# Kernel tuning notes

Measured on AMD Instinct MI355X. Metric: run time of the kernel, lower is better.

Reference implementation:

```python
import jax, jax.numpy as jnp
import numpy as np

NEG_INF = -9e15


def setup_inputs() -> dict:
    key = jax.random.key(0)
    k1, k2, k3, k4, k5 = jax.random.split(key, 5)
    N, F_IN, F_OUT = 8192, 512, 256
    x = jax.random.normal(k1, (N, F_IN), dtype=jnp.float32)
    adjacent_matrix = jax.random.randint(k2, (N, N), 0, 2, dtype=jnp.int32)
    # xavier-normal-like scales (gain sqrt(2))
    W = jax.random.normal(k3, (F_IN, F_OUT), dtype=jnp.float32) * np.sqrt(2.0) * np.sqrt(2.0 / (F_IN + F_OUT))
    a1 = jax.random.normal(k4, (F_OUT, 1), dtype=jnp.float32) * np.sqrt(2.0) * np.sqrt(2.0 / (F_OUT + 1))
    a2 = jax.random.normal(k5, (F_OUT, 1), dtype=jnp.float32) * np.sqrt(2.0) * np.sqrt(2.0 / (F_OUT + 1))
    return {"x": x, "adjacent_matrix": adjacent_matrix, "W": W, "a1": a1, "a2": a2}


def reference(x, adjacent_matrix, W, a1, a2):
    alpha = 0.2  # LeakyReLU negative slope
    h = x @ W                                   # [N, F_out]
    f1 = h @ a1                                 # [N, 1]
    f2 = h @ a2                                 # [N, 1]
    e = f1 + f2.T                               # [N, N] broadcast pairwise scores
    e = jnp.where(e > 0, e, alpha * e)          # LeakyReLU
    e = jnp.where(adjacent_matrix > 0, e, NEG_INF)  # mask non-edges
    attention = jax.nn.softmax(e, axis=1)       # [N, N]
    h_prime = attention @ h                     # [N, F_out]
    return jax.nn.elu(h_prime)                  # concat=True -> ELU
```

## Files before the change

### kernel.cpp

```cpp
#include <hip/hip_runtime.h>
#include <hip/hip_bf16.h>

#define N_NODES 8192
#define F_IN 512
#define F_OUT 256
#define KSPLIT 4
#define KCHUNK (N_NODES / KSPLIT)
#define NTILES (KCHUNK / 32)

using short8 = __attribute__((ext_vector_type(8))) short;
using f32x4  = __attribute__((ext_vector_type(4))) float;

typedef __attribute__((address_space(3))) void lds_t;
typedef const __attribute__((address_space(1))) void gbl_t;

__device__ __forceinline__ short f2bf(float v) {
    union { float f; unsigned u; } x; x.f = v;
    unsigned r = x.u + 0x7fffu + ((x.u >> 16) & 1u);
    return (short)(r >> 16);
}

__global__ void k_prep(const float* __restrict__ W, const float* __restrict__ a1,
                       const float* __restrict__ a2, float* __restrict__ w1,
                       float* __restrict__ w2, short* __restrict__ WTg) {
    const int k = blockIdx.x;
    const int l = threadIdx.x;
    float4 wv = *(const float4*)(W + (size_t)k * F_OUT + 4 * l);
    float4 av = *(const float4*)(a1 + 4 * l);
    float4 bv = *(const float4*)(a2 + 4 * l);
    float s1 = wv.x*av.x + wv.y*av.y + wv.z*av.z + wv.w*av.w;
    float s2 = wv.x*bv.x + wv.y*bv.y + wv.z*bv.z + wv.w*bv.w;
    WTg[(size_t)(4*l+0)*F_IN + k] = f2bf(wv.x);
    WTg[(size_t)(4*l+1)*F_IN + k] = f2bf(wv.y);
    WTg[(size_t)(4*l+2)*F_IN + k] = f2bf(wv.z);
    WTg[(size_t)(4*l+3)*F_IN + k] = f2bf(wv.w);
    #pragma unroll
    for (int off = 32; off; off >>= 1) {
        s1 += __shfl_down(s1, off);
        s2 += __shfl_down(s2, off);
    }
    if (l == 0) { w1[k] = s1; w2[k] = s2; }
}

__global__ void k_f12(const float* __restrict__ x, const float* __restrict__ w1,
                      const float* __restrict__ w2, float* __restrict__ f1,
                      float* __restrict__ f2) {
    const int wv = threadIdx.x >> 6, l = threadIdx.x & 63;
    const int i = blockIdx.x * 4 + wv;
    const float* xr = x + (size_t)i * F_IN;
    float s1 = 0.f, s2 = 0.f;
    #pragma unroll
    for (int t = 0; t < 2; ++t) {
        int k = t * 256 + l * 4;
        float4 xv = *(const float4*)(xr + k);
        float4 u  = *(const float4*)(w1 + k);
        float4 v  = *(const float4*)(w2 + k);
        s1 += xv.x*u.x + xv.y*u.y + xv.z*u.z + xv.w*u.w;
        s2 += xv.x*v.x + xv.y*v.y + xv.z*v.z + xv.w*v.w;
    }
    #pragma unroll
    for (int off = 32; off; off >>= 1) {
        s1 += __shfl_down(s1, off);
        s2 += __shfl_down(s2, off);
    }
    if (l == 0) { f1[i] = s1; f2[i] = s2; }
}

__launch_bounds__(256)
__global__ void k_hT(const float* __restrict__ x, const short* __restrict__ WTg,
                     short* __restrict__ hT) {
    __shared__ short x_lds[32 * 64];
    __shared__ short wt_lds[256 * 64];
    const int tid = threadIdx.x;
    const int wv = tid >> 6, l = tid & 63, lg = l >> 4, lr = l & 15;
    const int ibase = blockIdx.x * 32;
    f32x4 acc[4][2];
    #pragma unroll
    for (int a = 0; a < 4; ++a)
        #pragma unroll
        for (int b = 0; b < 2; ++b) acc[a][b] = (f32x4){0.f, 0.f, 0.f, 0.f};
    for (int k0 = 0; k0 < F_IN; k0 += 64) {
        __syncthreads();
        {
            int i = tid >> 3, ch = tid & 7;
            const float* src = x + (size_t)(ibase + i) * F_IN + k0 + ch * 8;
            float4 v0 = *(const float4*)(src);
            float4 v1 = *(const float4*)(src + 4);
            short8 s;
            s[0]=f2bf(v0.x); s[1]=f2bf(v0.y); s[2]=f2bf(v0.z); s[3]=f2bf(v0.w);
            s[4]=f2bf(v1.x); s[5]=f2bf(v1.y); s[6]=f2bf(v1.z); s[7]=f2bf(v1.w);
            *(short8*)&x_lds[i * 64 + 8 * (ch ^ (i & 7))] = s;
        }
        {
            int cb = tid >> 3, ch = tid & 7;
            #pragma unroll
            for (int p = 0; p < 8; ++p) {
                int c = cb + 32 * p;
                short8 s = *(const short8*)(WTg + (size_t)c * F_IN + k0 + ch * 8);
                *(short8*)&wt_lds[c * 64 + 8 * (ch ^ (c & 7))] = s;
            }
        }
        __syncthreads();
        #pragma unroll
        for (int ks = 0; ks < 2; ++ks) {
            short8 bfrag[2], afrag[4];
            #pragma unroll
            for (int it = 0; it < 2; ++it) {
                int i = it * 16 + lr;
                bfrag[it] = *(short8*)&x_lds[i * 64 + 8 * ((lg + 4*ks) ^ (i & 7))];
            }
            #pragma unroll
            for (int ct = 0; ct < 4; ++ct) {
                int c = wv * 64 + ct * 16 + lr;
                afrag[ct] = *(short8*)&wt_lds[c * 64 + 8 * ((lg + 4*ks) ^ (c & 7))];
            }
            #pragma unroll
            for (int ct = 0; ct < 4; ++ct)
                #pragma unroll
                for (int it = 0; it < 2; ++it)
                    acc[ct][it] = __builtin_amdgcn_mfma_f32_16x16x32_bf16(
                        afrag[ct], bfrag[it], acc[ct][it], 0, 0, 0);
        }
    }
    #pragma unroll
    for (int ct = 0; ct < 4; ++ct)
        #pragma unroll
        for (int it = 0; it < 2; ++it)
            #pragma unroll
            for (int r = 0; r < 4; ++r) {
                int c = wv * 64 + ct * 16 + 4 * lg + r;
                int i = ibase + it * 16 + lr;
                hT[(size_t)c * N_NODES + i] = f2bf(acc[ct][it][r]);
            }
}

__launch_bounds__(256, 2)
__global__ void k_attn(const int* __restrict__ adj, const short* __restrict__ hT,
                       const float* __restrict__ f1, const float* __restrict__ f2,
                       float* __restrict__ part, float* __restrict__ psum) {
    __shared__ short h_lds[4 * 8192];
    __shared__ float f2_lds[KCHUNK];
    const int tid = threadIdx.x;
    const int wv = tid >> 6, l = tid & 63, lg = l >> 4, lr = l & 15;
    const int ksid = blockIdx.x & 3;
    const int rowblk = blockIdx.x >> 2;
    const int r0 = rowblk * 64;
    const int myrow = r0 + wv * 16 + lr;
    const int kbeg = ksid * KCHUNK;
    const short* hsrcb = hT + (size_t)(wv * 16 + (l >> 2)) * N_NODES
                            + ((l & 3) ^ ((l >> 3) & 3)) * 8 + kbeg;
    const int q = l & 3, srow = wv * 16 + (l >> 2);
    const int* asrcb = adj + (size_t)(r0 + srow) * N_NODES + q * 8 + kbeg;
    const float f1v = f1[myrow];
    const float L2E = 1.44269504f;
    const int rdoff = lr * 32 + (lg ^ ((lr >> 1) & 3)) * 8;
    f32x4 acc[16];
    #pragma unroll
    for (int t = 0; t < 16; ++t) acc[t] = (f32x4){0.f, 0.f, 0.f, 0.f};
    float ps = 0.f;

    int4 S0[2], S1[2], S2[2], S3[2];
    unsigned mA, mB;

#define STAGE(T) do {                                                           \
    _Pragma("unroll")                                                           \
    for (int p = 0; p < 4; ++p)                                                 \
        __builtin_amdgcn_global_load_lds(                                       \
            (gbl_t*)(hsrcb + (size_t)p * 64 * N_NODES + (T) * 32),              \
            (lds_t*)&h_lds[((T) & 3) * 8192 + p * 2048 + wv * 512], 16, 0, 0);  \
} while (0)

#define ADJ(S, T) do {                                                          \
    S[0] = *(const int4*)(asrcb + (T) * 32);                                    \
    S[1] = *(const int4*)(asrcb + (T) * 32 + 4);                                \
} while (0)

#define PACK(MD, S) do {                                                        \
    unsigned _m = (S[0].x > 0 ? 1u : 0u) | (S[0].y > 0 ? 2u : 0u) |             \
                  (S[0].z > 0 ? 4u : 0u) | (S[0].w > 0 ? 8u : 0u) |             \
                  (S[1].x > 0 ? 16u : 0u) | (S[1].y > 0 ? 32u : 0u) |           \
                  (S[1].z > 0 ? 64u : 0u) | (S[1].w > 0 ? 128u : 0u);           \
    MD = (unsigned)__shfl((int)_m, (lr << 2) | lg);                             \
} while (0)

#define COMPUTE(T, MB) do {                                                     \
    const int bo = ((T) & 3) * 8192;                                            \
    const float4 fa = *(const float4*)&f2_lds[(T) * 32 + lg * 8];               \
    const float4 fb4 = *(const float4*)&f2_lds[(T) * 32 + lg * 8 + 4];          \
    const float f2v[8] = {fa.x, fa.y, fa.z, fa.w, fb4.x, fb4.y, fb4.z, fb4.w};  \
    short8 pa;                                                                  \
    _Pragma("unroll")                                                           \
    for (int j = 0; j < 8; ++j) {                                               \
        float ee = f1v + f2v[j];                                                \
        float le = fmaxf(ee, 0.2f * ee);                                        \
        float pv = ((MB) & (1u << j)) ? exp2f(fminf(le * L2E, 80.f)) : 0.f;     \
        ps += pv;                                                               \
        pa[j] = f2bf(pv);                                                       \
    }                                                                           \
    __builtin_amdgcn_s_setprio(1);                                              \
    _Pragma("unroll")                                                           \
    for (int t16 = 0; t16 < 16; ++t16) {                                        \
        short8 bfrag = *(short8*)&h_lds[bo + t16 * 512 + rdoff];                \
        acc[t16] = __builtin_amdgcn_mfma_f32_16x16x32_bf16(pa, bfrag, acc[t16], 0, 0, 0); \
    }                                                                           \
    __builtin_amdgcn_s_setprio(0);                                              \
} while (0)

#define BODY(T, SL, SP, MU, MP) do {                                            \
    PACK(MP, SP);                                        \
    if ((T) + 4 < NTILES) ADJ(SL, (T) + 4);                                     \
    if ((T) + 2 < NTILES) STAGE((T) + 2);                                       \
    asm volatile("s_waitcnt vmcnt(12)" ::: "memory");                           \
    __builtin_amdgcn_s_barrier();                                               \
    __builtin_amdgcn_sched_barrier(0);                                          \
    COMPUTE(T, MU);                                                             \
} while (0)

    {
        int i8 = tid * 8;
        *(float4*)&f2_lds[i8]     = *(const float4*)(f2 + kbeg + i8);
        *(float4*)&f2_lds[i8 + 4] = *(const float4*)(f2 + kbeg + i8 + 4);
    }
    ADJ(S0, 0); ADJ(S1, 1); ADJ(S2, 2); ADJ(S3, 3);
    STAGE(0); STAGE(1);
    PACK(mA, S0);
    __syncthreads();

    for (int t = 0; t < NTILES; t += 4) {
        BODY(t + 0, S0, S1, mA, mB);
        BODY(t + 1, S1, S2, mB, mA);
        BODY(t + 2, S2, S3, mA, mB);
        BODY(t + 3, S3, S0, mB, mA);
    }
#undef STAGE
#undef ADJ
#undef PACK
#undef COMPUTE
#undef BODY

    ps += __shfl_xor(ps, 16);
    ps += __shfl_xor(ps, 32);
    if (lg == 0) psum[ksid * N_NODES + myrow] = ps;
    float* pb = part + (size_t)ksid * N_NODES * F_OUT;
    #pragma unroll
    for (int t = 0; t < 16; ++t)
        #pragma unroll
        for (int r = 0; r < 4; ++r) {
            int row = r0 + wv * 16 + 4 * lg + r;
            int c = t * 16 + lr;
            pb[(size_t)row * F_OUT + c] = acc[t][r];
        }
}

__global__ void k_comb(const float* __restrict__ part, const float* __restrict__ psum,
                       float* __restrict__ out) {
    const int i = blockIdx.x, c = threadIdx.x;
    float o = 0.f, s = 0.f;
    #pragma unroll
    for (int qq = 0; qq < KSPLIT; ++qq) {
        o += part[(size_t)qq * N_NODES * F_OUT + (size_t)i * F_OUT + c];
        s += psum[qq * N_NODES + i];
    }
    float v = o / s;
    out[(size_t)i * F_OUT + c] = (v > 0.f) ? v : expm1f(v);
}

extern "C" void kernel_launch(void* const* d_in, const int* in_sizes, int n_in,
                              void* d_out, int out_size, void* d_ws, size_t ws_size,
                              hipStream_t stream) {
    const float* x  = (const float*)d_in[0];
    const int* adj  = (const int*)d_in[1];
    const float* W  = (const float*)d_in[2];
    const float* a1 = (const float*)d_in[3];
    const float* a2 = (const float*)d_in[4];
    float* out = (float*)d_out;

    short* hT  = (short*)d_ws;
    short* WTg = hT + (size_t)F_OUT * N_NODES;
    float* fb  = (float*)(WTg + (size_t)F_OUT * F_IN);
    float* w1   = fb;
    float* w2   = fb + 512;
    float* f1   = fb + 1024;
    float* f2   = fb + 1024 + N_NODES;
    float* part = fb + 32768;
    float* psum = part + (size_t)KSPLIT * N_NODES * F_OUT;

    k_prep<<<F_IN, 64, 0, stream>>>(W, a1, a2, w1, w2, WTg);
    k_f12<<<N_NODES / 4, 256, 0, stream>>>(x, w1, w2, f1, f2);
    k_hT<<<N_NODES / 32, 256, 0, stream>>>(x, WTg, hT);
    k_attn<<<128 * KSPLIT, 256, 0, stream>>>(adj, hT, f1, f2, part, psum);
    k_comb<<<N_NODES, 256, 0, stream>>>(part, psum, out);
}
```

Measured before the change: 437.9 us.

## Double rows per wave in attention kernel and raise K-split to eight

Each wave now handles two 16-row tiles (128 rows per block), so every h fragment read from LDS feeds two MFMAs. This halves the LDS and global traffic for hT per output row. KSPLIT goes from 4 to 8 to keep the grid at 512 blocks, and the prefetch depth for adjacency drops from four tiles to two, with a peeled epilogue for the last two tiles. In exchange, register use doubles for the accumulators, and the partial-sum buffer and the k_comb reduction both get larger.

```diff
diff --git a/kernel.cpp b/kernel.cpp
--- a/kernel.cpp
+++ b/kernel.cpp
@@ -4,9 +4,10 @@
 #define N_NODES 8192
 #define F_IN 512
 #define F_OUT 256
-#define KSPLIT 4
+#define KSPLIT 8
 #define KCHUNK (N_NODES / KSPLIT)
 #define NTILES (KCHUNK / 32)
+#define ROWSB 128
 
 using short8 = __attribute__((ext_vector_type(8))) short;
 using f32x4  = __attribute__((ext_vector_type(4))) float;
@@ -142,24 +143,27 @@
     __shared__ float f2_lds[KCHUNK];
     const int tid = threadIdx.x;
     const int wv = tid >> 6, l = tid & 63, lg = l >> 4, lr = l & 15;
-    const int ksid = blockIdx.x & 3;
-    const int rowblk = blockIdx.x >> 2;
-    const int r0 = rowblk * 64;
-    const int myrow = r0 + wv * 16 + lr;
+    const int ksid = blockIdx.x & 7;
+    const int rowblk = blockIdx.x >> 3;
+    const int r0 = rowblk * ROWSB;
+    const int row0 = r0 + wv * 32 + lr;
+    const int row1 = row0 + 16;
     const int kbeg = ksid * KCHUNK;
-    const short* hsrcb = hT + (size_t)(wv * 16 + (l >> 2)) * N_NODES
-                            + ((l & 3) ^ ((l >> 3) & 3)) * 8 + kbeg;
-    const int q = l & 3, srow = wv * 16 + (l >> 2);
-    const int* asrcb = adj + (size_t)(r0 + srow) * N_NODES + q * 8 + kbeg;
-    const float f1v = f1[myrow];
+    const short* hsrcb = hT + (size_t)(wv * 16 + (l >> 2)) * N_NODES + kbeg
+                            + ((l & 3) ^ ((l >> 2) & 3)) * 8;
+    const int* asrcb = adj + (size_t)(r0 + wv * 32 + (l >> 1)) * N_NODES + kbeg + (l & 1) * 16;
+    const float f1v0 = f1[row0];
+    const float f1v1 = f1[row1];
     const float L2E = 1.44269504f;
-    const int rdoff = lr * 32 + (lg ^ ((lr >> 1) & 3)) * 8;
-    f32x4 acc[16];
-    #pragma unroll
-    for (int t = 0; t < 16; ++t) acc[t] = (f32x4){0.f, 0.f, 0.f, 0.f};
-    float ps = 0.f;
-
-    int4 S0[2], S1[2], S2[2], S3[2];
+    f32x4 acc0[16], acc1[16];
+    #pragma unroll
+    for (int t = 0; t < 16; ++t) {
+        acc0[t] = (f32x4){0.f, 0.f, 0.f, 0.f};
+        acc1[t] = (f32x4){0.f, 0.f, 0.f, 0.f};
+    }
+    float ps0 = 0.f, ps1 = 0.f;
+
+    int4 SA[4], SB[4];
     unsigned mA, mB;
 
 #define STAGE(T) do {                                                           \
@@ -173,64 +177,84 @@
 #define ADJ(S, T) do {                                                          \
     S[0] = *(const int4*)(asrcb + (T) * 32);                                    \
     S[1] = *(const int4*)(asrcb + (T) * 32 + 4);                                \
+    S[2] = *(const int4*)(asrcb + (T) * 32 + 8);                                \
+    S[3] = *(const int4*)(asrcb + (T) * 32 + 12);                               \
 } while (0)
 
 #define PACK(MD, S) do {                                                        \
-    unsigned _m = (S[0].x > 0 ? 1u : 0u) | (S[0].y > 0 ? 2u : 0u) |             \
-                  (S[0].z > 0 ? 4u : 0u) | (S[0].w > 0 ? 8u : 0u) |             \
-                  (S[1].x > 0 ? 16u : 0u) | (S[1].y > 0 ? 32u : 0u) |           \
-                  (S[1].z > 0 ? 64u : 0u) | (S[1].w > 0 ? 128u : 0u);           \
-    MD = (unsigned)__shfl((int)_m, (lr << 2) | lg);                             \
-} while (0)
-
-#define COMPUTE(T, MB) do {                                                     \
+    unsigned _m = 0;                                                            \
+    _Pragma("unroll")                                                           \
+    for (int qq = 0; qq < 4; ++qq) {                                            \
+        _m |= (S[qq].x > 0 ? 1u : 0u) << (qq * 4);                              \
+        _m |= (S[qq].y > 0 ? 2u : 0u) << (qq * 4);                              \
+        _m |= (S[qq].z > 0 ? 4u : 0u) << (qq * 4);                              \
+        _m |= (S[qq].w > 0 ? 8u : 0u) << (qq * 4);                              \
+    }                                                                           \
+    unsigned _a0 = (unsigned)__shfl((int)_m, (lr << 1) | (lg >> 1));            \
+    unsigned _a1 = (unsigned)__shfl((int)_m, ((16 + lr) << 1) | (lg >> 1));     \
+    MD = ((_a0 >> (8 * (lg & 1))) & 0xffu) |                                    \
+         (((_a1 >> (8 * (lg & 1))) & 0xffu) << 8);                              \
+} while (0)
+
+#define COMPUTE(T, MD) do {                                                     \
     const int bo = ((T) & 3) * 8192;                                            \
     const float4 fa = *(const float4*)&f2_lds[(T) * 32 + lg * 8];               \
     const float4 fb4 = *(const float4*)&f2_lds[(T) * 32 + lg * 8 + 4];          \
     const float f2v[8] = {fa.x, fa.y, fa.z, fa.w, fb4.x, fb4.y, fb4.z, fb4.w};  \
-    short8 pa;                                                                  \
+    short8 pa0, pa1;                                                            \
     _Pragma("unroll")                                                           \
     for (int j = 0; j < 8; ++j) {                                               \
-        float ee = f1v + f2v[j];                                                \
-        float le = fmaxf(ee, 0.2f * ee);                                        \
-        float pv = ((MB) & (1u << j)) ? exp2f(fminf(le * L2E, 80.f)) : 0.f;     \
-        ps += pv;                                                               \
-        pa[j] = f2bf(pv);                                                       \
+        float e0 = f1v0 + f2v[j];                                               \
+        float e1 = f1v1 + f2v[j];                                               \
+        float le0 = fmaxf(e0, 0.2f * e0);                                       \
+        float le1 = fmaxf(e1, 0.2f * e1);                                       \
+        float p0 = ((MD) & (1u << j)) ? exp2f(fminf(le0 * L2E, 80.f)) : 0.f;    \
+        float p1 = ((MD) & (256u << j)) ? exp2f(fminf(le1 * L2E, 80.f)) : 0.f;  \
+        ps0 += p0; ps1 += p1;                                                   \
+        pa0[j] = f2bf(p0); pa1[j] = f2bf(p1);                                   \
     }                                                                           \
     __builtin_amdgcn_s_setprio(1);                                              \
     _Pragma("unroll")                                                           \
     for (int t16 = 0; t16 < 16; ++t16) {                                        \
-        short8 bfrag = *(short8*)&h_lds[bo + t16 * 512 + rdoff];                \
-        acc[t16] = __builtin_amdgcn_mfma_f32_16x16x32_bf16(pa, bfrag, acc[t16], 0, 0, 0); \
+        short8 bfrag = *(short8*)&h_lds[bo + t16 * 512 + lr * 32                \
+                                        + (lg ^ (lr & 3)) * 8];                 \
+        acc0[t16] = __builtin_amdgcn_mfma_f32_16x16x32_bf16(pa0, bfrag, acc0[t16], 0, 0, 0); \
+        acc1[t16] = __builtin_amdgcn_mfma_f32_16x16x32_bf16(pa1, bfrag, acc1[t16], 0, 0, 0); \
     }                                                                           \
     __builtin_amdgcn_s_setprio(0);                                              \
 } while (0)
 
-#define BODY(T, SL, SP, MU, MP) do {                                            \
-    PACK(MP, SP);                                        \
-    if ((T) + 4 < NTILES) ADJ(SL, (T) + 4);                                     \
-    if ((T) + 2 < NTILES) STAGE((T) + 2);                                       \
+#define BODY(T, SCUR, MCUR, SNXT, MNXT) do {                                    \
+    PACK(MNXT, SNXT);                                    \
+    ADJ(SCUR, (T) + 2);                                                         \
+    STAGE((T) + 2);                                                             \
     asm volatile("s_waitcnt vmcnt(12)" ::: "memory");                           \
     __builtin_amdgcn_s_barrier();                                               \
     __builtin_amdgcn_sched_barrier(0);                                          \
-    COMPUTE(T, MU);                                                             \
-} while (0)
-
+    COMPUTE(T, MCUR);                                                           \
+} while (0)
+
+    ADJ(SA, 0); ADJ(SB, 1);
+    STAGE(0); STAGE(1);
+    *(float4*)&f2_lds[tid * 4] = *(const float4*)(f2 + kbeg + tid * 4);
+    PACK(mA, SA);
+    __syncthreads();
+
+    for (int t = 0; t < NTILES - 2; t += 2) {
+        BODY(t,     SA, mA, SB, mB);
+        BODY(t + 1, SB, mB, SA, mA);
+    }
     {
-        int i8 = tid * 8;
-        *(float4*)&f2_lds[i8]     = *(const float4*)(f2 + kbeg + i8);
-        *(float4*)&f2_lds[i8 + 4] = *(const float4*)(f2 + kbeg + i8 + 4);
-    }
-    ADJ(S0, 0); ADJ(S1, 1); ADJ(S2, 2); ADJ(S3, 3);
-    STAGE(0); STAGE(1);
-    PACK(mA, S0);
-    __syncthreads();
-
-    for (int t = 0; t < NTILES; t += 4) {
-        BODY(t + 0, S0, S1, mA, mB);
-        BODY(t + 1, S1, S2, mB, mA);
-        BODY(t + 2, S2, S3, mA, mB);
-        BODY(t + 3, S3, S0, mB, mA);
+        PACK(mB, SB);
+        __builtin_amdgcn_s_barrier();
+        __builtin_amdgcn_sched_barrier(0);
+        COMPUTE(NTILES - 2, mA);
+    }
+    {
+        asm volatile("s_waitcnt vmcnt(0)" ::: "memory");
+        __builtin_amdgcn_s_barrier();
+        __builtin_amdgcn_sched_barrier(0);
+        COMPUTE(NTILES - 1, mB);
     }
 #undef STAGE
 #undef ADJ
@@ -238,17 +262,23 @@
 #undef COMPUTE
 #undef BODY
 
-    ps += __shfl_xor(ps, 16);
-    ps += __shfl_xor(ps, 32);
-    if (lg == 0) psum[ksid * N_NODES + myrow] = ps;
+    ps0 += __shfl_xor(ps0, 16);
+    ps0 += __shfl_xor(ps0, 32);
+    ps1 += __shfl_xor(ps1, 16);
+    ps1 += __shfl_xor(ps1, 32);
+    if (lg == 0) {
+        psum[ksid * N_NODES + row0] = ps0;
+        psum[ksid * N_NODES + row1] = ps1;
+    }
     float* pb = part + (size_t)ksid * N_NODES * F_OUT;
     #pragma unroll
     for (int t = 0; t < 16; ++t)
         #pragma unroll
         for (int r = 0; r < 4; ++r) {
-            int row = r0 + wv * 16 + 4 * lg + r;
             int c = t * 16 + lr;
-            pb[(size_t)row * F_OUT + c] = acc[t][r];
+            int rr0 = r0 + wv * 32 + 4 * lg + r;
+            pb[(size_t)rr0 * F_OUT + c] = acc0[t][r];
+            pb[(size_t)(rr0 + 16) * F_OUT + c] = acc1[t][r];
         }
 }
 
@@ -288,6 +318,6 @@
     k_prep<<<F_IN, 64, 0, stream>>>(W, a1, a2, w1, w2, WTg);
     k_f12<<<N_NODES / 4, 256, 0, stream>>>(x, w1, w2, f1, f2);
     k_hT<<<N_NODES / 32, 256, 0, stream>>>(x, WTg, hT);
-    k_attn<<<128 * KSPLIT, 256, 0, stream>>>(adj, hT, f1, f2, part, psum);
+    k_attn<<<(N_NODES / ROWSB) * KSPLIT, 256, 0, stream>>>(adj, hT, f1, f2, part, psum);
     k_comb<<<N_NODES, 256, 0, stream>>>(part, psum, out);
 }
```

Result: slower. 480.9 us (+9.8%).
